# Kernel optimization log

Measured on AMD Instinct MI355X. Metric: run time of the kernel, lower is better.

Reference implementation:

```python
import jax, jax.numpy as jnp
import numpy as np

CELLSIZE2 = (2e-9) ** 2  # cellsize ** 2 from __init__


def setup_inputs() -> dict:
    key = jax.random.key(0)
    k1, _ = jax.random.split(key)
    x = jax.random.normal(k1, (3, 512, 512, 64), dtype=jnp.float32)  # (3, Nx, Ny, Nz) spin field
    geo = jnp.ones((512, 512, 64), dtype=jnp.float32)  # geometry mask (unused by forward, kept for signature fidelity)
    D = jnp.array([1e-3], dtype=jnp.float32)  # DMI constant parameter, shape (1,) as in nn.Parameter(torch.tensor([D]))
    return {"x": x, "geo": geo, "D": D}


def reference(x, geo, D):
    # pbc=False: zero-pad the three spatial dims by 1 on each side
    xp = jnp.pad(x, ((0, 0), (1, 1), (1, 1), (1, 1)))
    roll = lambda s, a: jnp.roll(xp, shift=s, axis=a)
    # cross products over the component axis (axis 0), picking one component each
    d1 = jnp.cross(xp, roll(1, 1), axis=0)[1]
    d2 = -jnp.cross(xp, roll(-1, 1), axis=0)[1]
    d3 = -jnp.cross(xp, roll(1, 2), axis=0)[0]
    d4 = jnp.cross(xp, roll(-1, 2), axis=0)[0]
    E = (d1 + d2 + d3 + d4)[1:-1, 1:-1, 1:-1]  # crop padding -> (Nx, Ny, Nz)
    E = 0.5 * D[0] * CELLSIZE2 * E
    return jnp.mean(E)
```

## Files before the change

### kernel.cpp

```cpp
#include <hip/hip_runtime.h>

#define NX 512
#define NY 512
#define NZ 64
#define NCELL (NX * NY * NZ)
#define NG4   (NX * NY * (NZ / 4))
#define STRIDE_X (NY * NZ)
#define STRIDE_Y (NZ)

typedef float f4 __attribute__((ext_vector_type(4)));


__global__ __launch_bounds__(256) void dmi_partial(const float* __restrict__ x,
                                                   float* __restrict__ ws) {
    const float* mx = x;
    const float* my = x + NCELL;
    const float* mz = x + 2 * NCELL;

    float acc = 0.0f;
    int tid = blockIdx.x * blockDim.x + threadIdx.x;
    int nthreads = gridDim.x * blockDim.x;

    for (int g = tid; g < NG4; g += nthreads) {
        int iz4 = g & 15;
        int iy  = (g >> 4) & 511;
        int ix  = g >> 13;
        int off = (ix << 15) + (iy << 6) + (iz4 << 2);

        f4 ax = *(const f4*)(mx + off);
        f4 ay = *(const f4*)(my + off);
        f4 az = *(const f4*)(mz + off);

        f4 t = (f4)(0.0f);
        if (ix > 0) {
            f4 bx = *(const f4*)(mx + off - STRIDE_X);
            f4 bz = *(const f4*)(mz + off - STRIDE_X);
            t += az * bx - ax * bz;
        }
        if (iy > 0) {
            f4 by = *(const f4*)(my + off - STRIDE_Y);
            f4 bz = *(const f4*)(mz + off - STRIDE_Y);
            t += az * by - ay * bz;
        }
        acc += t[0] + t[1] + t[2] + t[3];
    }

    for (int o = 32; o > 0; o >>= 1) acc += __shfl_down(acc, o);

    __shared__ float sacc[4];
    int lane = threadIdx.x & 63;
    int wid  = threadIdx.x >> 6;
    if (lane == 0) sacc[wid] = acc;
    __syncthreads();
    if (threadIdx.x == 0)
        ws[blockIdx.x] = sacc[0] + sacc[1] + sacc[2] + sacc[3];
}

__global__ __launch_bounds__(256) void dmi_final(const float* __restrict__ ws,
                                                 const float* __restrict__ D,
                                                 float* __restrict__ out,
                                                 int nblocks) {
    double acc = 0.0;
    for (int i = threadIdx.x; i < nblocks; i += 256) acc += (double)ws[i];

    for (int o = 32; o > 0; o >>= 1) acc += __shfl_down(acc, o);

    __shared__ double sacc[4];
    int lane = threadIdx.x & 63;
    int wid  = threadIdx.x >> 6;
    if (lane == 0) sacc[wid] = acc;
    __syncthreads();
    if (threadIdx.x == 0) {
        double total = sacc[0] + sacc[1] + sacc[2] + sacc[3];
        double scale = (double)D[0] * 4e-18 / (double)NCELL;
        out[0] = (float)(total * scale);
    }
}

extern "C" void kernel_launch(void* const* d_in, const int* in_sizes, int n_in,
                              void* d_out, int out_size, void* d_ws, size_t ws_size,
                              hipStream_t stream) {
    const float* x = (const float*)d_in[0];
    const float* D = (const float*)d_in[2];
    float* out = (float*)d_out;
    float* ws  = (float*)d_ws;

    int nblocks = 2048;
    size_t avail = ws_size / sizeof(float);
    if ((size_t)nblocks > avail) nblocks = (int)(avail > 0 ? avail : 1);

    dmi_partial<<<nblocks, 256, 0, stream>>>(x, ws);
    dmi_final<<<1, 256, 0, stream>>>(ws, D, out, nblocks);
}
```

Before: 40.36 us.

## Fuse final reduction via last-block counter and reuse x-neighbour along per-thread runs

Each thread now walks a run of 8 consecutive x-planes and carries the previous plane's x and z components in registers, so the x-direction neighbour is no longer loaded from memory a second time. The separate final-reduction kernel is replaced by a last-block-done pattern: an atomic counter, cleared by a memset before launch, lets the last block sum the per-block partials and write the result. This trades one kernel launch for a memset node and atomic traffic, and relies on the workspace having room for the counter past the partials.

```diff
diff --git a/kernel.cpp b/kernel.cpp
--- a/kernel.cpp
+++ b/kernel.cpp
@@ -4,76 +4,89 @@
 #define NY 512
 #define NZ 64
 #define NCELL (NX * NY * NZ)
-#define NG4   (NX * NY * (NZ / 4))
-#define STRIDE_X (NY * NZ)
-#define STRIDE_Y (NZ)
+#define SX (NY * NZ)
+#define SY (NZ)
+#define LRUN 8
+#define NBLK 2048
 
 typedef float f4 __attribute__((ext_vector_type(4)));
 
 
-__global__ __launch_bounds__(256) void dmi_partial(const float* __restrict__ x,
-                                                   float* __restrict__ ws) {
+__global__ __launch_bounds__(256) void dmi_fused(const float* __restrict__ x,
+                                                 const float* __restrict__ D,
+                                                 float* __restrict__ out,
+                                                 float* __restrict__ ws,
+                                                 unsigned int* __restrict__ counter) {
     const float* mx = x;
     const float* my = x + NCELL;
     const float* mz = x + 2 * NCELL;
 
+    int t   = blockIdx.x * 256 + threadIdx.x;
+    int iz4 = t & 15;
+    int iy  = (t >> 4) & 511;
+    int cx  = t >> 13;
+    int off = cx * (LRUN * SX) + iy * SY + (iz4 << 2);
+
+    f4 px, pz;
+    if (cx > 0) {
+        px = *(const f4*)(mx + off - SX);
+        pz = *(const f4*)(mz + off - SX);
+    } else {
+        px = (f4)(0.0f);
+        pz = (f4)(0.0f);
+    }
+
+    const bool has_y = (iy > 0);
     float acc = 0.0f;
-    int tid = blockIdx.x * blockDim.x + threadIdx.x;
-    int nthreads = gridDim.x * blockDim.x;
-
-    for (int g = tid; g < NG4; g += nthreads) {
-        int iz4 = g & 15;
-        int iy  = (g >> 4) & 511;
-        int ix  = g >> 13;
-        int off = (ix << 15) + (iy << 6) + (iz4 << 2);
-
+#pragma unroll
+    for (int j = 0; j < LRUN; ++j, off += SX) {
         f4 ax = *(const f4*)(mx + off);
         f4 ay = *(const f4*)(my + off);
         f4 az = *(const f4*)(mz + off);
-
-        f4 t = (f4)(0.0f);
-        if (ix > 0) {
-            f4 bx = *(const f4*)(mx + off - STRIDE_X);
-            f4 bz = *(const f4*)(mz + off - STRIDE_X);
-            t += az * bx - ax * bz;
+        f4 tv = az * px - ax * pz;
+        if (has_y) {
+            f4 by = *(const f4*)(my + off - SY);
+            f4 bz = *(const f4*)(mz + off - SY);
+            tv += az * by - ay * bz;
         }
-        if (iy > 0) {
-            f4 by = *(const f4*)(my + off - STRIDE_Y);
-            f4 bz = *(const f4*)(mz + off - STRIDE_Y);
-            t += az * by - ay * bz;
-        }
-        acc += t[0] + t[1] + t[2] + t[3];
+        acc += tv[0] + tv[1] + tv[2] + tv[3];
+        px = ax;
+        pz = az;
     }
 
     for (int o = 32; o > 0; o >>= 1) acc += __shfl_down(acc, o);
 
     __shared__ float sacc[4];
+    __shared__ int lastFlag;
     int lane = threadIdx.x & 63;
     int wid  = threadIdx.x >> 6;
     if (lane == 0) sacc[wid] = acc;
     __syncthreads();
-    if (threadIdx.x == 0)
-        ws[blockIdx.x] = sacc[0] + sacc[1] + sacc[2] + sacc[3];
-}
 
-__global__ __launch_bounds__(256) void dmi_final(const float* __restrict__ ws,
-                                                 const float* __restrict__ D,
-                                                 float* __restrict__ out,
-                                                 int nblocks) {
-    double acc = 0.0;
-    for (int i = threadIdx.x; i < nblocks; i += 256) acc += (double)ws[i];
+    if (threadIdx.x == 0) {
+        float p = sacc[0] + sacc[1] + sacc[2] + sacc[3];
+        atomicExch(&ws[blockIdx.x], p);
+        __threadfence();
+        unsigned prev = atomicAdd(counter, 1u);
+        lastFlag = (prev == NBLK - 1) ? 1 : 0;
+    }
+    __syncthreads();
 
-    for (int o = 32; o > 0; o >>= 1) acc += __shfl_down(acc, o);
+    if (lastFlag) {
+        __threadfence();
+        double d = 0.0;
+        for (int i = threadIdx.x; i < NBLK; i += 256)
+            d += (double)atomicAdd(&ws[i], 0.0f);
+        for (int o = 32; o > 0; o >>= 1) d += __shfl_down(d, o);
 
-    __shared__ double sacc[4];
-    int lane = threadIdx.x & 63;
-    int wid  = threadIdx.x >> 6;
-    if (lane == 0) sacc[wid] = acc;
-    __syncthreads();
-    if (threadIdx.x == 0) {
-        double total = sacc[0] + sacc[1] + sacc[2] + sacc[3];
-        double scale = (double)D[0] * 4e-18 / (double)NCELL;
-        out[0] = (float)(total * scale);
+        __shared__ double dacc[4];
+        if (lane == 0) dacc[wid] = d;
+        __syncthreads();
+        if (threadIdx.x == 0) {
+            double total = dacc[0] + dacc[1] + dacc[2] + dacc[3];
+            double scale = (double)D[0] * 4e-18 / (double)NCELL;
+            out[0] = (float)(total * scale);
+        }
     }
 }
 
@@ -84,11 +97,8 @@
     const float* D = (const float*)d_in[2];
     float* out = (float*)d_out;
     float* ws  = (float*)d_ws;
+    unsigned int* counter = (unsigned int*)((char*)d_ws + NBLK * sizeof(float));
 
-    int nblocks = 2048;
-    size_t avail = ws_size / sizeof(float);
-    if ((size_t)nblocks > avail) nblocks = (int)(avail > 0 ? avail : 1);
-
-    dmi_partial<<<nblocks, 256, 0, stream>>>(x, ws);
-    dmi_final<<<1, 256, 0, stream>>>(ws, D, out, nblocks);
+    hipMemsetAsync(counter, 0, sizeof(unsigned int), stream);
+    dmi_fused<<<NBLK, 256, 0, stream>>>(x, D, out, ws, counter);
 }
```

Measured after the change: 110.1 us. +172.8%, slower.
